# Optimization experiments

Hardware: AMD Instinct MI355X
Metric: run time of the kernel (lower is better)

## Reference

```python
import jax, jax.numpy as jnp
import numpy as np

VOCAB_SIZE = 4096
D_EMBED = 256
BETA = 0.25  # unused: module returns raw commit_loss; beta applied by caller


def setup_inputs() -> dict:
    key = jax.random.key(0)
    k_h, k_e = jax.random.split(key)
    h = jax.random.normal(k_h, (16, D_EMBED, 32, 32), dtype=jnp.float32)
    embedding = jax.random.normal(k_e, (VOCAB_SIZE, D_EMBED), dtype=jnp.float32)
    return {"h": h, "embedding": embedding}


def reference(h, embedding):
    B, C, H, W = h.shape
    h = h.astype(jnp.float32)
    # (B, C, H, W) -> (N, C) with N = B*H*W
    h_flat = jnp.transpose(h, (0, 2, 3, 1)).reshape(-1, C)
    dist = (
        jnp.sum(h_flat * h_flat, axis=1, keepdims=True)
        + jnp.sum(embedding * embedding, axis=1)
        - 2.0 * jnp.einsum("nc,vc->nv", h_flat, embedding)
    )
    indices_flat = jnp.argmin(dist, axis=1)
    indices = indices_flat.reshape(B, H, W)
    # gather codebook vectors and restore (B, C, H, W)
    z_q = jnp.transpose(embedding[indices_flat].reshape(B, H, W, C), (0, 3, 1, 2))
    commit_loss = jnp.mean((h - jax.lax.stop_gradient(z_q)) ** 2)
    # straight-through estimator
    z_q_st = h + jax.lax.stop_gradient(z_q - h)
    return z_q_st, indices, commit_loss
```

## Files before the change

### kernel.cpp

```cpp
#include <hip/hip_runtime.h>

#define D 256
#define VOCAB 4096
#define NTOT 16384
#define N_OUT0 4194304

typedef _Float16 half8 __attribute__((ext_vector_type(8)));
typedef float f32x4 __attribute__((ext_vector_type(4)));

__device__ __forceinline__ void gld16(const void* g, void* l) {
    __builtin_amdgcn_global_load_lds(
        (const __attribute__((address_space(1))) void*)g,
        (__attribute__((address_space(3))) void*)l, 16, 0, 0);
}

__device__ __forceinline__ unsigned long long pack_key(float d, int v) {
    unsigned u = __float_as_uint(d);
    u ^= ((unsigned)((int)u >> 31)) | 0x80000000u;
    return ((unsigned long long)u << 32) | (unsigned)v;
}

__global__ __launch_bounds__(256) void k_pack(const float* __restrict__ h,
                                              const float* __restrict__ emb,
                                              _Float16* __restrict__ Apk,
                                              _Float16* __restrict__ Bpk,
                                              float* __restrict__ esq,
                                              unsigned long long* __restrict__ gbest,
                                              float* __restrict__ out2) {
    __shared__ float S[8192];
    const int tid = threadIdx.x;
    const int bid = blockIdx.x;
    if (bid < 512) {
        const int bm = bid >> 3, w = bid & 7;
        const int b = bm >> 2, p0 = (bm & 3) * 256;
        const float* src = h + ((size_t)b << 18) + p0;
#pragma unroll 4
        for (int cl = 0; cl < 32; ++cl)
            S[cl * 256 + tid] = src[(size_t)(w * 32 + cl) << 10 | (unsigned)tid];
        __syncthreads();
        _Float16* dstT = Apk + (size_t)bm * 131072 + (size_t)w * 16384;
#pragma unroll
        for (int i = 0; i < 4; ++i) {
            alignas(16) _Float16 hi[8], lo[8];
#pragma unroll
            for (int j = 0; j < 8; ++j) {
                float vv = S[(i * 8 + j) * 256 + tid];
                _Float16 hv = (_Float16)vv;
                hi[j] = hv;
                lo[j] = (_Float16)(vv - (float)hv);
            }
            _Float16* dst = dstT + i * 2048 + tid * 8;
            *(half8*)dst = *(half8*)hi;
            *(half8*)(dst + 8192) = *(half8*)lo;
        }
    } else if (bid < 768) {
        const int bid2 = bid - 512;
        const int bn = bid2 >> 3, w = bid2 & 7;
        const int v0 = bn * 128;
#pragma unroll 4
        for (int i = 0; i < 16; ++i) {
            int flat = i * 256 + tid;
            int r = flat >> 5, cl = flat & 31;
            S[cl * 129 + r] = emb[(size_t)(v0 + r) * D + w * 32 + cl];
        }
        __syncthreads();
        _Float16* dstT = Bpk + (size_t)bn * 65536 + (size_t)w * 8192;
#pragma unroll
        for (int i = 0; i < 2; ++i) {
            int s = i * 256 + tid;
            int q = s >> 7, r = s & 127;
            alignas(16) _Float16 hi[8], lo[8];
#pragma unroll
            for (int j = 0; j < 8; ++j) {
                float vv = S[(q * 8 + j) * 129 + r];
                _Float16 hv = (_Float16)vv;
                hi[j] = hv;
                lo[j] = (_Float16)(vv - (float)hv);
            }
            _Float16* dst = dstT + q * 1024 + r * 8;
            *(half8*)dst = *(half8*)hi;
            *(half8*)(dst + 4096) = *(half8*)lo;
        }
    } else {
        const int pid = bid - 768;
        const int lane = tid & 63, wv = tid >> 6;
#pragma unroll 4
        for (int i = 0; i < 16; ++i) {
            int v = pid * 64 + i * 4 + wv;
            float4 e = *(const float4*)(emb + (size_t)v * D + lane * 4);
            float s = e.x * e.x + e.y * e.y + e.z * e.z + e.w * e.w;
#pragma unroll
            for (int m = 32; m >= 1; m >>= 1) s += __shfl_xor(s, m, 64);
            if (lane == 0) esq[v] = s;
        }
        gbest[pid * 256 + tid] = ~0ULL;
        if (pid == 0 && tid == 0) out2[0] = 0.0f;
    }
}


#define STAGE_ALL(W, NB) do { \
    const _Float16* sa_ = Ag + (W) * 16384; \
    const _Float16* sb0_ = Bg0 + (W) * 8192; \
    const _Float16* sb1_ = Bg1 + (W) * 8192; \
    gld16(sa_ + tid * 8, As + (NB) + tid * 8); \
    gld16(sa_ + 4096 + tid * 8, As + (NB) + 4096 + tid * 8); \
    gld16(sa_ + 8192 + tid * 8, As + (NB) + 8192 + tid * 8); \
    gld16(sa_ + 12288 + tid * 8, As + (NB) + 12288 + tid * 8); \
    gld16(sb0_ + tid * 8, Bs + (NB) + tid * 8); \
    gld16(sb0_ + 4096 + tid * 8, Bs + (NB) + 4096 + tid * 8); \
    gld16(sb1_ + tid * 8, Bs + (NB) + 8192 + tid * 8); \
    gld16(sb1_ + 4096 + tid * 8, Bs + (NB) + 12288 + tid * 8); \
} while (0)

#define LOAD_AF(OFF) do { _Pragma("unroll") \
    for (int mt_ = 0; mt_ < 8; ++mt_) af[mt_] = *(const half8*)(aB + (OFF) + mt_ * 128); } while (0)
#define LOAD_BF(OFF) do { _Pragma("unroll") \
    for (int nt_ = 0; nt_ < 4; ++nt_) bf[nt_] = *(const half8*)(bB + (OFF) + nt_ * 128); } while (0)

#define MFMA32() do { \
    __builtin_amdgcn_s_setprio(1); \
    _Pragma("unroll") \
    for (int mt_ = 0; mt_ < 8; ++mt_) { \
      _Pragma("unroll") \
      for (int nt_ = 0; nt_ < 4; ++nt_) \
        acc[mt_][nt_] = __builtin_amdgcn_mfma_f32_16x16x32_f16(af[mt_], bf[nt_], acc[mt_][nt_], 0, 0, 0); \
    } \
    __builtin_amdgcn_s_setprio(0); \
  } while (0)

__global__ __launch_bounds__(512, 2) void k_gemm(const _Float16* __restrict__ Apk,
                                                 const _Float16* __restrict__ Bpk,
                                                 const float* __restrict__ esq,
                                                 unsigned long long* __restrict__ gbest) {
    __shared__ alignas(16) _Float16 As[32768];
    __shared__ alignas(16) _Float16 Bs[32768];

    const int tid = threadIdx.x;
    const int bid = blockIdx.x;
    const int swz = (bid & 7) * 128 + (bid >> 3);
    const int bm = swz >> 4, bn = swz & 15;
    const int m0 = bm * 256, n0 = bn * 256;

    const _Float16* Ag = Apk + (size_t)bm * 131072;
    const _Float16* Bg0 = Bpk + (size_t)(2 * bn) * 65536;
    const _Float16* Bg1 = Bpk + (size_t)(2 * bn + 1) * 65536;

    STAGE_ALL(0, 0);

    const int wv = tid >> 6, l = tid & 63;
    const int wm = wv & 1, wn = wv >> 1;
    const int quad = l >> 4, j16 = l & 15;
    const int arow = wm * 128 + j16;
    const int brow = (wn & 1) * 64 + j16;
    const int bsub = wn >> 1;

    f32x4 acc[8][4];
#pragma unroll
    for (int i = 0; i < 8; ++i)
#pragma unroll
        for (int j = 0; j < 4; ++j) acc[i][j] = (f32x4)0.0f;

    __syncthreads();

#pragma unroll 1
    for (int w = 0; w < 8; ++w) {
        const int cb = (w & 1) << 14, nb = cb ^ 16384;
        const _Float16* aB = As + cb + quad * 2048 + arow * 8;
        const _Float16* bB = Bs + cb + bsub * 8192 + quad * 1024 + brow * 8;
        if (w < 7) STAGE_ALL(w + 1, nb);
        half8 af[8], bf[4];
        LOAD_AF(0);
        LOAD_BF(4096);
        MFMA32();
        LOAD_BF(0);
        MFMA32();
        LOAD_AF(8192);
        MFMA32();
        __syncthreads();
    }

    unsigned long long* red = (unsigned long long*)As;
    if (tid < 256) red[tid] = ~0ULL;
    __syncthreads();

    float es[4];
#pragma unroll
    for (int nt = 0; nt < 4; ++nt) es[nt] = esq[n0 + wn * 64 + nt * 16 + j16];
#pragma unroll
    for (int mt = 0; mt < 8; ++mt) {
#pragma unroll
        for (int r = 0; r < 4; ++r) {
            unsigned long long best = ~0ULL;
#pragma unroll
            for (int nt = 0; nt < 4; ++nt) {
                float dv = es[nt] - 2.0f * acc[mt][nt][r];
                unsigned long long key = pack_key(dv, n0 + wn * 64 + nt * 16 + j16);
                best = key < best ? key : best;
            }
#pragma unroll
            for (int m = 8; m >= 1; m >>= 1) {
                unsigned long long o = __shfl_xor(best, m, 64);
                best = o < best ? o : best;
            }
            if (j16 == 0) atomicMin(&red[wm * 128 + mt * 16 + quad * 4 + r], best);
        }
    }
    __syncthreads();
    if (tid < 256) atomicMin(&gbest[m0 + tid], red[tid]);
}

__global__ __launch_bounds__(256) void k_gather(const float* __restrict__ h,
                                                const float* __restrict__ emb,
                                                const unsigned long long* __restrict__ gbest,
                                                float* __restrict__ out0,
                                                float* __restrict__ out1,
                                                float* __restrict__ out2) {
    __shared__ float zq[32][260];
    __shared__ float wred[4];
    const int tid = threadIdx.x;
    const int lane = tid & 63;
    const int w = tid >> 6;
    const int n0 = blockIdx.x * 32;
    const int b = n0 >> 10;
    const int p0 = n0 & 1023;
#pragma unroll
    for (int rr = 0; rr < 8; ++rr) {
        int r = w * 8 + rr;
        unsigned idx = (unsigned)(gbest[n0 + r] & 0xFFFFFFFFULL);
        float4 e4 = *(const float4*)(emb + (size_t)idx * D + lane * 4);
        *(float4*)&zq[r][lane * 4] = e4;
    }
    if (tid < 32) {
        unsigned idx = (unsigned)(gbest[n0 + tid] & 0xFFFFFFFFULL);
        out1[n0 + tid] = (float)idx;
    }
    __syncthreads();
    float lsum = 0.0f;
    const size_t base = ((size_t)b * D) << 10;
#pragma unroll 4
    for (int it = 0; it < 32; ++it) {
        int c = it * 8 + (tid >> 5);
        int pp = tid & 31;
        float z = zq[pp][c];
        size_t g = base + ((size_t)c << 10) + p0 + pp;
        float hv = h[g];
        out0[g] = hv + (z - hv);
        float d = hv - z;
        lsum = fmaf(d, d, lsum);
    }
#pragma unroll
    for (int m = 32; m >= 1; m >>= 1) lsum += __shfl_xor(lsum, m, 64);
    if (lane == 0) wred[w] = lsum;
    __syncthreads();
    if (tid == 0)
        atomicAdd(out2, (wred[0] + wred[1] + wred[2] + wred[3]) * (1.0f / (float)N_OUT0));
}

extern "C" void kernel_launch(void* const* d_in, const int* in_sizes, int n_in,
                              void* d_out, int out_size, void* d_ws, size_t ws_size,
                              hipStream_t stream) {
    const float* h = (const float*)d_in[0];
    const float* emb = (const float*)d_in[1];
    float* out0 = (float*)d_out;
    float* out1 = out0 + N_OUT0;
    float* out2 = out1 + NTOT;

    _Float16* Apk = (_Float16*)d_ws;
    _Float16* Bpk = (_Float16*)((char*)d_ws + 16777216);
    float* esq = (float*)((char*)d_ws + 16777216 + 4194304);
    unsigned long long* gbest = (unsigned long long*)((char*)d_ws + 16777216 + 4194304 + 16384);

    hipLaunchKernelGGL(k_pack, dim3(832), dim3(256), 0, stream, h, emb, Apk, Bpk, esq, gbest, out2);
    hipLaunchKernelGGL(k_gemm, dim3(1024), dim3(512), 0, stream, Apk, Bpk, esq, gbest);
    hipLaunchKernelGGL(k_gather, dim3(NTOT / 32), dim3(256), 0, stream, h, emb, gbest, out0, out1, out2);
}
```

Measured before the change: 201.1 us.

## Shrink GEMM tile to 128x128 with single-buffered A and more blocks

Reduces the distance GEMM block tile from 256x256 with 512 threads to 128x128 with 256 threads, launching 4096 blocks at up to 3 per CU. A stays single-buffered and is restaged mid-iteration behind an extra barrier, while B stays double-buffered. The aim is higher occupancy and better load balance across CUs. In exchange, each block reuses its staged data less, global/L2 traffic for A and B roughly doubles, there is one more sync per k-step, and twice as many atomicMin calls hit gbest.

```diff
diff --git a/kernel.cpp b/kernel.cpp
--- a/kernel.cpp
+++ b/kernel.cpp
@@ -99,29 +99,27 @@
 }
 
 
-#define STAGE_ALL(W, NB) do { \
-    const _Float16* sa_ = Ag + (W) * 16384; \
-    const _Float16* sb0_ = Bg0 + (W) * 8192; \
-    const _Float16* sb1_ = Bg1 + (W) * 8192; \
-    gld16(sa_ + tid * 8, As + (NB) + tid * 8); \
-    gld16(sa_ + 4096 + tid * 8, As + (NB) + 4096 + tid * 8); \
-    gld16(sa_ + 8192 + tid * 8, As + (NB) + 8192 + tid * 8); \
-    gld16(sa_ + 12288 + tid * 8, As + (NB) + 12288 + tid * 8); \
-    gld16(sb0_ + tid * 8, Bs + (NB) + tid * 8); \
-    gld16(sb0_ + 4096 + tid * 8, Bs + (NB) + 4096 + tid * 8); \
-    gld16(sb1_ + tid * 8, Bs + (NB) + 8192 + tid * 8); \
-    gld16(sb1_ + 4096 + tid * 8, Bs + (NB) + 12288 + tid * 8); \
-} while (0)
+#define STAGE_A(W) do { _Pragma("unroll") \
+    for (int it_ = 0; it_ < 4; ++it_) { \
+        int f_ = it_ * 256 + tid; \
+        gld16(AgH + (W) * 16384 + (f_ >> 9) * 8192 + ((f_ >> 7) & 3) * 2048 + (f_ & 127) * 8, \
+              As + f_ * 8); \
+    } } while (0)
+#define STAGE_B(W, NB) do { _Pragma("unroll") \
+    for (int it_ = 0; it_ < 4; ++it_) { \
+        int f_ = it_ * 256 + tid; \
+        gld16(Bg + (W) * 8192 + f_ * 8, Bs + (NB) + f_ * 8); \
+    } } while (0)
 
 #define LOAD_AF(OFF) do { _Pragma("unroll") \
-    for (int mt_ = 0; mt_ < 8; ++mt_) af[mt_] = *(const half8*)(aB + (OFF) + mt_ * 128); } while (0)
+    for (int mt_ = 0; mt_ < 4; ++mt_) af[mt_] = *(const half8*)(aB + (OFF) + mt_ * 128); } while (0)
 #define LOAD_BF(OFF) do { _Pragma("unroll") \
     for (int nt_ = 0; nt_ < 4; ++nt_) bf[nt_] = *(const half8*)(bB + (OFF) + nt_ * 128); } while (0)
 
-#define MFMA32() do { \
+#define MFMA16() do { \
     __builtin_amdgcn_s_setprio(1); \
     _Pragma("unroll") \
-    for (int mt_ = 0; mt_ < 8; ++mt_) { \
+    for (int mt_ = 0; mt_ < 4; ++mt_) { \
       _Pragma("unroll") \
       for (int nt_ = 0; nt_ < 4; ++nt_) \
         acc[mt_][nt_] = __builtin_amdgcn_mfma_f32_16x16x32_f16(af[mt_], bf[nt_], acc[mt_][nt_], 0, 0, 0); \
@@ -129,35 +127,33 @@
     __builtin_amdgcn_s_setprio(0); \
   } while (0)
 
-__global__ __launch_bounds__(512, 2) void k_gemm(const _Float16* __restrict__ Apk,
+__global__ __launch_bounds__(256, 3) void k_gemm(const _Float16* __restrict__ Apk,
                                                  const _Float16* __restrict__ Bpk,
                                                  const float* __restrict__ esq,
                                                  unsigned long long* __restrict__ gbest) {
-    __shared__ alignas(16) _Float16 As[32768];
-    __shared__ alignas(16) _Float16 Bs[32768];
+    __shared__ alignas(16) _Float16 As[8192];
+    __shared__ alignas(16) _Float16 Bs[16384];
 
     const int tid = threadIdx.x;
     const int bid = blockIdx.x;
-    const int swz = (bid & 7) * 128 + (bid >> 3);
-    const int bm = swz >> 4, bn = swz & 15;
-    const int m0 = bm * 256, n0 = bn * 256;
-
-    const _Float16* Ag = Apk + (size_t)bm * 131072;
-    const _Float16* Bg0 = Bpk + (size_t)(2 * bn) * 65536;
-    const _Float16* Bg1 = Bpk + (size_t)(2 * bn + 1) * 65536;
-
-    STAGE_ALL(0, 0);
+    const int swz = (bid & 7) * 512 + (bid >> 3);
+    const int bm = swz >> 5, bn = swz & 31;
+    const int m0 = bm * 128, n0 = bn * 128;
+
+    const _Float16* AgH = Apk + (size_t)(bm >> 1) * 131072 + (size_t)(bm & 1) * 1024;
+    const _Float16* Bg = Bpk + (size_t)bn * 65536;
+
+    STAGE_A(0);
+    STAGE_B(0, 0);
 
     const int wv = tid >> 6, l = tid & 63;
     const int wm = wv & 1, wn = wv >> 1;
     const int quad = l >> 4, j16 = l & 15;
-    const int arow = wm * 128 + j16;
-    const int brow = (wn & 1) * 64 + j16;
-    const int bsub = wn >> 1;
-
-    f32x4 acc[8][4];
-#pragma unroll
-    for (int i = 0; i < 8; ++i)
+    const _Float16* aB = As + quad * 1024 + (wm * 64 + j16) * 8;
+
+    f32x4 acc[4][4];
+#pragma unroll
+    for (int i = 0; i < 4; ++i)
 #pragma unroll
         for (int j = 0; j < 4; ++j) acc[i][j] = (f32x4)0.0f;
 
@@ -165,37 +161,44 @@
 
 #pragma unroll 1
     for (int w = 0; w < 8; ++w) {
-        const int cb = (w & 1) << 14, nb = cb ^ 16384;
-        const _Float16* aB = As + cb + quad * 2048 + arow * 8;
-        const _Float16* bB = Bs + cb + bsub * 8192 + quad * 1024 + brow * 8;
-        if (w < 7) STAGE_ALL(w + 1, nb);
-        half8 af[8], bf[4];
+        const int cb = (w & 1) << 13, nb = cb ^ 8192;
+        const _Float16* bB = Bs + cb + quad * 1024 + (wn * 64 + j16) * 8;
+        if (w < 7) STAGE_B(w + 1, nb);
+        half8 af[4], bf[4];
         LOAD_AF(0);
         LOAD_BF(4096);
-        MFMA32();
+        MFMA16();
         LOAD_BF(0);
-        MFMA32();
-        LOAD_AF(8192);
-        MFMA32();
+        MFMA16();
+        LOAD_AF(4096);
+        if (w < 7) {
+            __syncthreads();
+            STAGE_A(w + 1);
+        }
+        MFMA16();
         __syncthreads();
     }
 
     unsigned long long* red = (unsigned long long*)As;
-    if (tid < 256) red[tid] = ~0ULL;
+    if (tid < 128) red[tid] = ~0ULL;
     __syncthreads();
 
     float es[4];
-#pragma unroll
-    for (int nt = 0; nt < 4; ++nt) es[nt] = esq[n0 + wn * 64 + nt * 16 + j16];
-#pragma unroll
-    for (int mt = 0; mt < 8; ++mt) {
+    int vidx[4];
+#pragma unroll
+    for (int nt = 0; nt < 4; ++nt) {
+        vidx[nt] = n0 + wn * 64 + nt * 16 + j16;
+        es[nt] = esq[vidx[nt]];
+    }
+#pragma unroll
+    for (int mt = 0; mt < 4; ++mt) {
 #pragma unroll
         for (int r = 0; r < 4; ++r) {
             unsigned long long best = ~0ULL;
 #pragma unroll
             for (int nt = 0; nt < 4; ++nt) {
                 float dv = es[nt] - 2.0f * acc[mt][nt][r];
-                unsigned long long key = pack_key(dv, n0 + wn * 64 + nt * 16 + j16);
+                unsigned long long key = pack_key(dv, vidx[nt]);
                 best = key < best ? key : best;
             }
 #pragma unroll
@@ -203,11 +206,11 @@
                 unsigned long long o = __shfl_xor(best, m, 64);
                 best = o < best ? o : best;
             }
-            if (j16 == 0) atomicMin(&red[wm * 128 + mt * 16 + quad * 4 + r], best);
-        }
-    }
-    __syncthreads();
-    if (tid < 256) atomicMin(&gbest[m0 + tid], red[tid]);
+            if (j16 == 0) atomicMin(&red[wm * 64 + mt * 16 + quad * 4 + r], best);
+        }
+    }
+    __syncthreads();
+    if (tid < 128) atomicMin(&gbest[m0 + tid], red[tid]);
 }
 
 __global__ __launch_bounds__(256) void k_gather(const float* __restrict__ h,
@@ -272,6 +275,6 @@
     unsigned long long* gbest = (unsigned long long*)((char*)d_ws + 16777216 + 4194304 + 16384);
 
     hipLaunchKernelGGL(k_pack, dim3(832), dim3(256), 0, stream, h, emb, Apk, Bpk, esq, gbest, out2);
-    hipLaunchKernelGGL(k_gemm, dim3(1024), dim3(512), 0, stream, Apk, Bpk, esq, gbest);
+    hipLaunchKernelGGL(k_gemm, dim3(4096), dim3(256), 0, stream, Apk, Bpk, esq, gbest);
     hipLaunchKernelGGL(k_gather, dim3(NTOT / 32), dim3(256), 0, stream, h, emb, gbest, out0, out1, out2);
 }
```

Result: no change. 202.7 us (+0.8%).
